# Kernel optimization log

Measured on AMD Instinct MI355X. Metric: run time of the kernel, lower is better.

The kernel has to match this reference:

```python
import jax, jax.numpy as jnp
import numpy as np

DIM = 512
WINDOW = 8
HEADS = 16
HEAD_DIM = DIM // HEADS
SIGMA = 0.39
B = 2048
N = WINDOW * WINDOW


def gaussian_kernel(window_size, sigma):
    """Row-normalised Gaussian attention mask K_sigma (M^2 x M^2)."""
    c = jnp.arange(window_size, dtype=jnp.float32)
    gy, gx = jnp.meshgrid(c, c, indexing='ij')
    pos = jnp.stack([gy.flatten(), gx.flatten()], -1)  # [M^2, 2]
    diff = pos[None, :, :] - pos[:, None, :]           # [M^2, M^2, 2]
    K = jnp.exp(-(diff ** 2).sum(-1) / (2.0 * sigma ** 2))
    return K / K.sum(-1, keepdims=True)


def setup_inputs() -> dict:
    key = jax.random.key(0)
    k1, k2, k3, k4, k5 = jax.random.split(key, 5)
    x = jax.random.normal(k1, (B, N, DIM), dtype=jnp.float32)
    # spectral_norm at inference is just a fixed scaling of the weight; we
    # model the (already-normalised) weights as plain dense params.
    w_qkv = jax.random.normal(k2, (DIM, 3 * DIM), dtype=jnp.float32) * (DIM ** -0.5)
    b_qkv = jax.random.normal(k3, (3 * DIM,), dtype=jnp.float32) * 0.02
    w_proj = jax.random.normal(k4, (DIM, DIM), dtype=jnp.float32) * (DIM ** -0.5)
    b_proj = jax.random.normal(k5, (DIM,), dtype=jnp.float32) * 0.02
    return {"x": x, "w_qkv": w_qkv, "b_qkv": b_qkv, "w_proj": w_proj, "b_proj": b_proj}


def reference(x, w_qkv, b_qkv, w_proj, b_proj):
    Bb, Nn, C = x.shape
    scale = HEAD_DIM ** -0.5
    qkv = (x @ w_qkv + b_qkv).reshape(Bb, Nn, 3, HEADS, HEAD_DIM)
    qkv = jnp.transpose(qkv, (2, 0, 3, 1, 4))  # [3, B, H, N, D]
    q, k, v = qkv[0], qkv[1], qkv[2]
    attn = jnp.einsum('bhnd,bhmd->bhnm', q, k) * scale  # [B, H, N, N]
    K_s = gaussian_kernel(WINDOW, SIGMA)                 # [N, N]
    attn = jax.nn.softmax(attn * K_s, axis=-1)
    out = jnp.einsum('bhnm,bhmd->bhnd', attn, v)         # [B, H, N, D]
    out = jnp.transpose(out, (0, 2, 1, 3)).reshape(Bb, Nn, C)
    return out @ w_proj + b_proj
```

## Files before the change

kernel.cpp:

```cpp
#include <hip/hip_runtime.h>
#include <hip/hip_bf16.h>
#include <stdint.h>

typedef __bf16 bf16;
typedef __bf16 bf16x8 __attribute__((ext_vector_type(8)));
typedef float f32x4 __attribute__((ext_vector_type(4)));
typedef unsigned short u16t;
typedef unsigned int u32t;

#define MFMA16(a, b, c) __builtin_amdgcn_mfma_f32_16x16x32_bf16((a), (b), (c), 0, 0, 0)

typedef const void __attribute__((address_space(1))) cg_void;
typedef void __attribute__((address_space(3))) lds_void;
#define GLL16(g, l) __builtin_amdgcn_global_load_lds((cg_void*)(g), (lds_void*)(l), 16, 0, 0)

#define OFF_FLAG   0
#define OFF_BQKV   256
#define OFF_BPROJ  6400
#define OFF_WQKVT  8448
#define OFF_WPROJT 1581312
#define OFF_QKV    2105600
#define OFF_ATTN   404758784

__global__ __launch_bounds__(256) void k_detect(const u16t* x, u32t* flag) {
    __shared__ int cnt;
    if (threadIdx.x == 0) cnt = 0;
    __syncthreads();
    u16t h = x[threadIdx.x * 2];
    int e = (h >> 7) & 0xFF;
    int ok = (h == 0) || (e >= 100 && e <= 134);
    atomicAdd(&cnt, ok);
    __syncthreads();
    if (threadIdx.x == 0) flag[0] = (cnt >= 200) ? 1u : 0u;
}

template <int N>
__global__ __launch_bounds__(256) void k_trans(const void* W, bf16* Wt, const u32t* flagp) {
    __shared__ float T[64][65];
    const int isbf = (int)flagp[0];
    const int n0 = blockIdx.x * 64, k0 = blockIdx.y * 64;
    const int t = threadIdx.x;
    const int lc = t & 63, lr = t >> 6;
#pragma unroll
    for (int rr = 0; rr < 16; ++rr) {
        int row = rr * 4 + lr;
        size_t g = (size_t)(k0 + row) * N + n0 + lc;
        float v = isbf ? (float)((const bf16*)W)[g] : ((const float*)W)[g];
        T[row][lc] = v;
    }
    __syncthreads();
#pragma unroll
    for (int rr = 0; rr < 16; ++rr) {
        int row = rr * 4 + lr;
        Wt[(size_t)(n0 + row) * 512 + k0 + lc] = (bf16)T[lc][row];
    }
}

__global__ __launch_bounds__(256) void k_bias(const void* b_qkv, const void* b_proj,
                                              const u32t* flagp, char* ws) {
    float* bq = (float*)(ws + OFF_BQKV);
    float* bp = (float*)(ws + OFF_BPROJ);
    const int isbf = (int)flagp[0];
    int gid = blockIdx.x * 256 + threadIdx.x;
    if (gid < 1536)
        bq[gid] = isbf ? (float)((const bf16*)b_qkv)[gid] : ((const float*)b_qkv)[gid];
    else if (gid < 2048) {
        int o = gid - 1536;
        bp[o] = isbf ? (float)((const bf16*)b_proj)[o] : ((const float*)b_proj)[o];
    }
}

template <int NTOT>
__global__ __launch_bounds__(256) void k_gemm(const void* Ax, const bf16* Bt,
                                              const float* bias, void* Cp,
                                              const u32t* flagp, int amode, int omode) {
    __shared__ __align__(16) u16t As[8192];
    __shared__ __align__(16) u16t Bs[8192];
    constexpr int NBN = NTOT / 128;
    const int isbf = (int)flagp[0];
    const int a_is_f32 = (amode == 1) && !isbf;
    const int out_bf16 = (omode == 1) || isbf;

    const int t = threadIdx.x;
    const int w = t >> 6, lane = t & 63;
    const int ln = lane & 15, qd = lane >> 4;

    const int flat = blockIdx.x;
    const int xcd = flat & 7, slot = flat >> 3;
    const int n_idx = slot % NBN, grp = slot / NBN;
    const int m0 = (grp * 8 + xcd) * 128;
    const int n0 = n_idx * 128;
    const int wr = (w >> 1) * 64, wc = (w & 1) * 64;

    u32t aoff[4], boff[4];
    int physl[4];
#pragma unroll
    for (int q = 0; q < 4; ++q) {
        int phys = w * 256 + q * 64 + lane;
        int r = phys >> 3, c = (phys & 7) ^ (r & 7);
        physl[q] = phys;
        aoff[q] = (u32t)(m0 + r) * 512 + c * 8;
        boff[q] = (u32t)(n0 + r) * 512 + c * 8;
    }
    int aoffs[4], boffs[4];
#pragma unroll
    for (int i = 0; i < 4; ++i) {
        int ra = wr + i * 16 + ln;
        aoffs[i] = ((ra << 3) | (qd ^ (ra & 7))) * 8;
        int rb = wc + i * 16 + ln;
        boffs[i] = ((rb << 3) | (qd ^ (rb & 7))) * 8;
    }

    const bf16* Ab = (const bf16*)Ax;
    const float* Af = (const float*)Ax;

    f32x4 acc[4][4];
    f32x4 zero = {0.f, 0.f, 0.f, 0.f};
#pragma unroll
    for (int i = 0; i < 4; ++i)
#pragma unroll
        for (int j = 0; j < 4; ++j) acc[i][j] = zero;

    for (int kt = 0; kt < 8; ++kt) {
        if (a_is_f32) {
#pragma unroll
            for (int q = 0; q < 4; ++q) {
                float4 v0 = *(const float4*)(Af + aoff[q]);
                float4 v1 = *(const float4*)(Af + aoff[q] + 4);
                bf16x8 h;
                h[0] = (bf16)v0.x; h[1] = (bf16)v0.y; h[2] = (bf16)v0.z; h[3] = (bf16)v0.w;
                h[4] = (bf16)v1.x; h[5] = (bf16)v1.y; h[6] = (bf16)v1.z; h[7] = (bf16)v1.w;
                *(bf16x8*)(void*)&As[physl[q] * 8] = h;
            }
        } else {
#pragma unroll
            for (int q = 0; q < 4; ++q)
                GLL16(Ab + aoff[q], &As[(w * 256 + q * 64) * 8]);
        }
#pragma unroll
        for (int q = 0; q < 4; ++q)
            GLL16(Bt + boff[q], &Bs[(w * 256 + q * 64) * 8]);
        __syncthreads();
#pragma unroll
        for (int kk = 0; kk < 2; ++kk) {
            bf16x8 af[4], bfr[4];
#pragma unroll
            for (int i = 0; i < 4; ++i) af[i] = *(const bf16x8*)(void*)&As[aoffs[i] ^ (kk * 32)];
#pragma unroll
            for (int j = 0; j < 4; ++j) bfr[j] = *(const bf16x8*)(void*)&Bs[boffs[j] ^ (kk * 32)];
#pragma unroll
            for (int i = 0; i < 4; ++i)
#pragma unroll
                for (int j = 0; j < 4; ++j) acc[i][j] = MFMA16(af[i], bfr[j], acc[i][j]);
        }
        __syncthreads();
#pragma unroll
        for (int q = 0; q < 4; ++q) { aoff[q] += 64; boff[q] += 64; }
    }

    float bj[4];
#pragma unroll
    for (int j = 0; j < 4; ++j) bj[j] = bias[n0 + wc + j * 16 + ln];

    if (out_bf16) {
        bf16* C = (bf16*)Cp;
#pragma unroll
        for (int i = 0; i < 4; ++i)
#pragma unroll
            for (int j = 0; j < 4; ++j)
#pragma unroll
                for (int rr = 0; rr < 4; ++rr) {
                    size_t row = (size_t)m0 + wr + i * 16 + qd * 4 + rr;
                    int col = n0 + wc + j * 16 + ln;
                    C[row * NTOT + col] = (bf16)(acc[i][j][rr] + bj[j]);
                }
    } else {
        float* C = (float*)Cp;
#pragma unroll
        for (int i = 0; i < 4; ++i)
#pragma unroll
            for (int j = 0; j < 4; ++j)
#pragma unroll
                for (int rr = 0; rr < 4; ++rr) {
                    size_t row = (size_t)m0 + wr + i * 16 + qd * 4 + rr;
                    int col = n0 + wc + j * 16 + ln;
                    C[row * NTOT + col] = acc[i][j][rr] + bj[j];
                }
    }
}

__global__ __launch_bounds__(256) void k_attn(const bf16* qkv, bf16* attn) {
    __shared__ __align__(16) bf16 P[4][64 * 72];
    const int t = threadIdx.x;
    const int w = t >> 6, lane = t & 63;
    const int ln = lane & 15, qd = lane >> 4, q8 = qd * 8;
    const int flat = blockIdx.x;
    const int xcd = flat & 7, slot = flat >> 3;
    const int sub = slot & 3, grp = slot >> 2;
    const int b = grp * 8 + xcd;
    const int h = sub * 4 + w;
    const size_t rowbase = (size_t)b * 64 * 1536;
    const int colq = h * 32 + q8;

    bf16x8 aq[4], bk[4];
#pragma unroll
    for (int i = 0; i < 4; ++i)
        aq[i] = *(const bf16x8*)(qkv + rowbase + (size_t)(i * 16 + ln) * 1536 + colq);
#pragma unroll
    for (int j = 0; j < 4; ++j)
        bk[j] = *(const bf16x8*)(qkv + rowbase + (size_t)(j * 16 + ln) * 1536 + 512 + colq);

    f32x4 zero = {0.f, 0.f, 0.f, 0.f};
    f32x4 s[4][4];
#pragma unroll
    for (int i = 0; i < 4; ++i)
#pragma unroll
        for (int j = 0; j < 4; ++j) s[i][j] = MFMA16(aq[i], bk[j], zero);

    const float INV2S2 = 3.28731097961867f;
    {
        int c = lane & 7;
        float S1 = 0.f;
#pragma unroll
        for (int c2 = 0; c2 < 8; ++c2) {
            int d = c - c2;
            S1 += __expf(-(float)(d * d) * INV2S2);
        }
        float invS1 = 1.0f / S1;
        const int ymb = ln >> 3, xm = ln & 7, yq = qd >> 1, xq = (qd & 1) * 4;
        float FY[4][4], FX[4];
#pragma unroll
        for (int i = 0; i < 4; ++i) {
            int yn = 2 * i + yq;
            float g = __shfl(invS1, yn, 64);
#pragma unroll
            for (int j = 0; j < 4; ++j) {
                int dy = yn - (2 * j + ymb);
                FY[i][j] = __expf(-(float)(dy * dy) * INV2S2) * g;
            }
        }
#pragma unroll
        for (int rr = 0; rr < 4; ++rr) {
            int xn = xq + rr;
            int dx = xn - xm;
            FX[rr] = __expf(-(float)(dx * dx) * INV2S2) * __shfl(invS1, xn, 64);
        }

        const float SCALE = 0.17677669529663687f;
#pragma unroll
        for (int i = 0; i < 4; ++i)
#pragma unroll
            for (int rr = 0; rr < 4; ++rr) {
                float lj[4];
                float mx = -1e30f;
#pragma unroll
                for (int j = 0; j < 4; ++j) {
                    lj[j] = s[i][j][rr] * SCALE * FY[i][j] * FX[rr];
                    mx = fmaxf(mx, lj[j]);
                }
                mx = fmaxf(mx, __shfl_xor(mx, 1));
                mx = fmaxf(mx, __shfl_xor(mx, 2));
                mx = fmaxf(mx, __shfl_xor(mx, 4));
                mx = fmaxf(mx, __shfl_xor(mx, 8));
                float sum = 0.f;
#pragma unroll
                for (int j = 0; j < 4; ++j) {
                    lj[j] = __expf(lj[j] - mx);
                    sum += lj[j];
                }
                sum += __shfl_xor(sum, 1);
                sum += __shfl_xor(sum, 2);
                sum += __shfl_xor(sum, 4);
                sum += __shfl_xor(sum, 8);
                float inv = 1.0f / sum;
                int n = i * 16 + qd * 4 + rr;
#pragma unroll
                for (int j = 0; j < 4; ++j)
                    P[w][n * 72 + j * 16 + ln] = (bf16)(lj[j] * inv);
            }
    }

    f32x4 o[4][2];
#pragma unroll
    for (int i = 0; i < 4; ++i) {
        o[i][0] = zero;
        o[i][1] = zero;
    }
#pragma unroll
    for (int kc = 0; kc < 64; kc += 32) {
        bf16x8 bv[2];
#pragma unroll
        for (int j2 = 0; j2 < 2; ++j2)
#pragma unroll
            for (int jj = 0; jj < 8; ++jj)
                bv[j2][jj] = qkv[rowbase + (size_t)(kc + q8 + jj) * 1536 + 1024 + h * 32 + j2 * 16 + ln];
#pragma unroll
        for (int i = 0; i < 4; ++i) {
            bf16x8 ap = *(const bf16x8*)(void*)&P[w][(i * 16 + ln) * 72 + kc + q8];
#pragma unroll
            for (int j2 = 0; j2 < 2; ++j2) o[i][j2] = MFMA16(ap, bv[j2], o[i][j2]);
        }
    }
#pragma unroll
    for (int i = 0; i < 4; ++i)
#pragma unroll
        for (int j2 = 0; j2 < 2; ++j2)
#pragma unroll
            for (int rr = 0; rr < 4; ++rr)
                attn[((size_t)b * 64 + i * 16 + qd * 4 + rr) * 512 + h * 32 + j2 * 16 + ln] =
                    (bf16)(o[i][j2][rr]);
}

extern "C" void kernel_launch(void* const* d_in, const int* in_sizes, int n_in,
                              void* d_out, int out_size, void* d_ws, size_t ws_size,
                              hipStream_t stream) {
    const void* x = d_in[0];
    const void* w_qkv = d_in[1];
    const void* b_qkv = d_in[2];
    const void* w_proj = d_in[3];
    const void* b_proj = d_in[4];
    char* ws = (char*)d_ws;
    u32t* flag = (u32t*)(ws + OFF_FLAG);
    bf16* wqkvT = (bf16*)(ws + OFF_WQKVT);
    bf16* wprojT = (bf16*)(ws + OFF_WPROJT);
    float* bq = (float*)(ws + OFF_BQKV);
    float* bp = (float*)(ws + OFF_BPROJ);
    bf16* qkv = (bf16*)(ws + OFF_QKV);
    bf16* attn = (bf16*)(ws + OFF_ATTN);

    k_detect<<<1, 256, 0, stream>>>((const u16t*)x, flag);
    k_trans<1536><<<dim3(24, 8), 256, 0, stream>>>(w_qkv, wqkvT, flag);
    k_trans<512><<<dim3(8, 8), 256, 0, stream>>>(w_proj, wprojT, flag);
    k_bias<<<8, 256, 0, stream>>>(b_qkv, b_proj, flag, ws);
    k_gemm<1536><<<12288, 256, 0, stream>>>(x, wqkvT, bq, qkv, flag, 1, 1);
    k_attn<<<8192, 256, 0, stream>>>(qkv, attn);
    k_gemm<512><<<4096, 256, 0, stream>>>(attn, wprojT, bp, d_out, flag, 0, 2);
}
```

Measured before the change: 943.9 us.

## Pre-convert x to bf16 and double-buffer GEMM LDS staging with async loads

Adds a separate pass that converts the fp32 input x to bf16 in workspace, so the QKV GEMM can load A with async global-to-LDS copies instead of converting fp32 inline. The GEMM now double-buffers A and B tiles in LDS, issuing the next k-tile's loads before computing the current one, so memory latency overlaps with MFMA work. The cost is an extra full read and write of x, plus twice the LDS per block, which may reduce occupancy. The xb buffer shares its workspace offset with the attention output; this looks safe because xb is only read by the first GEMM, before attention writes there.

```diff
diff --git a/kernel.cpp b/kernel.cpp
--- a/kernel.cpp
+++ b/kernel.cpp
@@ -21,6 +21,7 @@
 #define OFF_WPROJT 1581312
 #define OFF_QKV    2105600
 #define OFF_ATTN   404758784
+#define OFF_XB     404758784
 
 __global__ __launch_bounds__(256) void k_detect(const u16t* x, u32t* flag) {
     __shared__ int cnt;
@@ -32,6 +33,21 @@
     atomicAdd(&cnt, ok);
     __syncthreads();
     if (threadIdx.x == 0) flag[0] = (cnt >= 200) ? 1u : 0u;
+}
+
+__global__ __launch_bounds__(256) void k_cvt(const float* x, bf16* xb, const u32t* flagp) {
+    if (flagp[0]) return;
+    const size_t TOT = (size_t)131072 * 512;
+    size_t i = (size_t)(blockIdx.x * 256 + threadIdx.x) * 8;
+    const size_t stride = (size_t)gridDim.x * 256 * 8;
+    for (; i < TOT; i += stride) {
+        float4 v0 = *(const float4*)(x + i);
+        float4 v1 = *(const float4*)(x + i + 4);
+        bf16x8 h;
+        h[0] = (bf16)v0.x; h[1] = (bf16)v0.y; h[2] = (bf16)v0.z; h[3] = (bf16)v0.w;
+        h[4] = (bf16)v1.x; h[5] = (bf16)v1.y; h[6] = (bf16)v1.z; h[7] = (bf16)v1.w;
+        *(bf16x8*)(xb + i) = h;
+    }
 }
 
 template <int N>
@@ -71,15 +87,15 @@
 }
 
 template <int NTOT>
-__global__ __launch_bounds__(256) void k_gemm(const void* Ax, const bf16* Bt,
+__global__ __launch_bounds__(256) void k_gemm(const void* Ax, const bf16* Axb, const bf16* Bt,
                                               const float* bias, void* Cp,
-                                              const u32t* flagp, int amode, int omode) {
-    __shared__ __align__(16) u16t As[8192];
-    __shared__ __align__(16) u16t Bs[8192];
+                                              const u32t* flagp, int omode) {
+    __shared__ __align__(16) u16t As[2][8192];
+    __shared__ __align__(16) u16t Bs[2][8192];
     constexpr int NBN = NTOT / 128;
     const int isbf = (int)flagp[0];
-    const int a_is_f32 = (amode == 1) && !isbf;
     const int out_bf16 = (omode == 1) || isbf;
+    const bf16* Ab = isbf ? (const bf16*)Ax : Axb;
 
     const int t = threadIdx.x;
     const int w = t >> 6, lane = t & 63;
@@ -93,12 +109,12 @@
     const int wr = (w >> 1) * 64, wc = (w & 1) * 64;
 
     u32t aoff[4], boff[4];
-    int physl[4];
+    int ldst[4];
 #pragma unroll
     for (int q = 0; q < 4; ++q) {
         int phys = w * 256 + q * 64 + lane;
         int r = phys >> 3, c = (phys & 7) ^ (r & 7);
-        physl[q] = phys;
+        ldst[q] = (w * 256 + q * 64) * 8;
         aoff[q] = (u32t)(m0 + r) * 512 + c * 8;
         boff[q] = (u32t)(n0 + r) * 512 + c * 8;
     }
@@ -111,9 +127,6 @@
         boffs[i] = ((rb << 3) | (qd ^ (rb & 7))) * 8;
     }
 
-    const bf16* Ab = (const bf16*)Ax;
-    const float* Af = (const float*)Ax;
-
     f32x4 acc[4][4];
     f32x4 zero = {0.f, 0.f, 0.f, 0.f};
 #pragma unroll
@@ -121,41 +134,41 @@
 #pragma unroll
         for (int j = 0; j < 4; ++j) acc[i][j] = zero;
 
-    for (int kt = 0; kt < 8; ++kt) {
-        if (a_is_f32) {
-#pragma unroll
-            for (int q = 0; q < 4; ++q) {
-                float4 v0 = *(const float4*)(Af + aoff[q]);
-                float4 v1 = *(const float4*)(Af + aoff[q] + 4);
-                bf16x8 h;
-                h[0] = (bf16)v0.x; h[1] = (bf16)v0.y; h[2] = (bf16)v0.z; h[3] = (bf16)v0.w;
-                h[4] = (bf16)v1.x; h[5] = (bf16)v1.y; h[6] = (bf16)v1.z; h[7] = (bf16)v1.w;
-                *(bf16x8*)(void*)&As[physl[q] * 8] = h;
-            }
-        } else {
-#pragma unroll
-            for (int q = 0; q < 4; ++q)
-                GLL16(Ab + aoff[q], &As[(w * 256 + q * 64) * 8]);
-        }
+    auto STAGE = [&](int buf, int kt) {
 #pragma unroll
         for (int q = 0; q < 4; ++q)
-            GLL16(Bt + boff[q], &Bs[(w * 256 + q * 64) * 8]);
-        __syncthreads();
+            GLL16(Ab + aoff[q] + kt * 64, &As[buf][ldst[q]]);
+#pragma unroll
+        for (int q = 0; q < 4; ++q)
+            GLL16(Bt + boff[q] + kt * 64, &Bs[buf][ldst[q]]);
+    };
+    auto COMPUTE = [&](int buf) {
 #pragma unroll
         for (int kk = 0; kk < 2; ++kk) {
             bf16x8 af[4], bfr[4];
 #pragma unroll
-            for (int i = 0; i < 4; ++i) af[i] = *(const bf16x8*)(void*)&As[aoffs[i] ^ (kk * 32)];
-#pragma unroll
-            for (int j = 0; j < 4; ++j) bfr[j] = *(const bf16x8*)(void*)&Bs[boffs[j] ^ (kk * 32)];
-#pragma unroll
             for (int i = 0; i < 4; ++i)
+                af[i] = *(const bf16x8*)(void*)&As[buf][aoffs[i] ^ (kk * 32)];
+#pragma unroll
+            for (int j = 0; j < 4; ++j)
+                bfr[j] = *(const bf16x8*)(void*)&Bs[buf][boffs[j] ^ (kk * 32)];
+#pragma unroll
+            for (int i = 0; i < 4; ++i)
 #pragma unroll
                 for (int j = 0; j < 4; ++j) acc[i][j] = MFMA16(af[i], bfr[j], acc[i][j]);
         }
+    };
+
+    STAGE(0, 0);
+    __syncthreads();
+#pragma unroll
+    for (int kt = 0; kt < 8; kt += 2) {
+        STAGE(1, kt + 1);
+        COMPUTE(0);
         __syncthreads();
-#pragma unroll
-        for (int q = 0; q < 4; ++q) { aoff[q] += 64; boff[q] += 64; }
+        if (kt + 2 < 8) STAGE(0, kt + 2);
+        COMPUTE(1);
+        __syncthreads();
     }
 
     float bj[4];
@@ -327,12 +340,14 @@
     float* bp = (float*)(ws + OFF_BPROJ);
     bf16* qkv = (bf16*)(ws + OFF_QKV);
     bf16* attn = (bf16*)(ws + OFF_ATTN);
+    bf16* xb = (bf16*)(ws + OFF_XB);
 
     k_detect<<<1, 256, 0, stream>>>((const u16t*)x, flag);
+    k_cvt<<<2048, 256, 0, stream>>>((const float*)x, xb, flag);
     k_trans<1536><<<dim3(24, 8), 256, 0, stream>>>(w_qkv, wqkvT, flag);
     k_trans<512><<<dim3(8, 8), 256, 0, stream>>>(w_proj, wprojT, flag);
     k_bias<<<8, 256, 0, stream>>>(b_qkv, b_proj, flag, ws);
-    k_gemm<1536><<<12288, 256, 0, stream>>>(x, wqkvT, bq, qkv, flag, 1, 1);
+    k_gemm<1536><<<12288, 256, 0, stream>>>(x, xb, wqkvT, bq, qkv, flag, 1);
     k_attn<<<8192, 256, 0, stream>>>(qkv, attn);
-    k_gemm<512><<<4096, 256, 0, stream>>>(attn, wprojT, bp, d_out, flag, 0, 2);
-}
+    k_gemm<512><<<4096, 256, 0, stream>>>((const void*)attn, attn, wprojT, bp, d_out, flag, 2);
+}
```

Result: slower. 1.045 ms (+10.7%).
